# Optimization experiments

Hardware: AMD Instinct MI355X
Metric: run time of the kernel (lower is better)

The kernel has to match this reference:

```python
import jax, jax.numpy as jnp
import numpy as np

G = 7          # 7x7 feature map -> 49 nodes per image
N = G * G
K = 3          # knn_k
NEG_SLOPE = 0.2  # PyG GATConv default leaky_relu slope


def build_spatial_edges():
    # 8-neighborhood grid edges on the 7x7 map, directed (src -> dst)
    src, dst = [], []
    for r in range(G):
        for c in range(G):
            i = r * G + c
            for dr in (-1, 0, 1):
                for dc in (-1, 0, 1):
                    if dr == 0 and dc == 0:
                        continue
                    rr, cc = r + dr, c + dc
                    if 0 <= rr < G and 0 <= cc < G:
                        src.append(rr * G + cc)
                        dst.append(i)
    return np.array([src, dst], dtype=np.int32)

SPATIAL = build_spatial_edges()  # [2, 312]


def build_edges(x):
    """x: [B, N, F] node features -> (src, dst) each [B, E].
    Edges = spatial 8-neighborhood + feature-space kNN (k=3) + self-loops."""
    B = x.shape[0]
    sq = jnp.sum(x * x, axis=-1)                               # [B, N]
    d = sq[:, :, None] + sq[:, None, :] - 2.0 * jnp.einsum('bnf,bmf->bnm', x, x)
    d = d + jnp.eye(N, dtype=x.dtype) * 1e9                    # exclude self
    _, nbr = jax.lax.top_k(-d, K)                              # [B, N, K]
    knn_src = nbr.reshape(B, N * K)
    knn_dst = jnp.broadcast_to(jnp.repeat(jnp.arange(N, dtype=jnp.int32), K)[None], (B, N * K))
    sp = jnp.asarray(SPATIAL)
    Es = sp.shape[1]
    loops = jnp.arange(N, dtype=jnp.int32)
    src = jnp.concatenate([jnp.broadcast_to(sp[0][None], (B, Es)), knn_src.astype(jnp.int32),
                           jnp.broadcast_to(loops[None], (B, N))], axis=1)
    dst = jnp.concatenate([jnp.broadcast_to(sp[1][None], (B, Es)), knn_dst,
                           jnp.broadcast_to(loops[None], (B, N))], axis=1)
    return src, dst


def gat_layer(x, src, dst, W, a_src, a_dst, b, concat):
    """PyG-style GATConv (eval mode, no dropout). x: [N,F], src/dst: [E]."""
    H, C = a_src.shape
    h = (x @ W).reshape(N, H, C)                               # [N, H, C]
    es = jnp.sum(h * a_src[None], axis=-1)                     # [N, H]
    ed = jnp.sum(h * a_dst[None], axis=-1)                     # [N, H]
    e = jax.nn.leaky_relu(es[src] + ed[dst], NEG_SLOPE)        # [E, H]
    m = jax.ops.segment_max(e, dst, num_segments=N)            # [N, H]
    m = jnp.where(jnp.isfinite(m), m, 0.0)
    p = jnp.exp(e - m[dst])
    denom = jax.ops.segment_sum(p, dst, num_segments=N)
    alpha = p / jnp.maximum(denom[dst], 1e-16)                 # softmax over incoming edges
    out = jax.ops.segment_sum(alpha[:, :, None] * h[src], dst, num_segments=N)  # [N, H, C]
    out = out.reshape(N, H * C) if concat else out.mean(axis=1)
    return out + b


def setup_inputs() -> dict:
    key = jax.random.key(0)
    ks = jax.random.split(key, 14)
    B, F, Hd, Cd, O, NC = 256, 1024, 8, 128, 256, 14
    s = 0.05
    return {
        'feat_map': jax.random.normal(ks[0], (B, F, G, G), dtype=jnp.float32),
        'W1': jax.random.normal(ks[1], (F, Hd * Cd), dtype=jnp.float32) * s,
        'a_src1': jax.random.normal(ks[2], (Hd, Cd), dtype=jnp.float32) * s,
        'a_dst1': jax.random.normal(ks[3], (Hd, Cd), dtype=jnp.float32) * s,
        'b1': jnp.zeros((Hd * Cd,), dtype=jnp.float32),
        'W2': jax.random.normal(ks[4], (Hd * Cd, O), dtype=jnp.float32) * s,
        'a_src2': jax.random.normal(ks[5], (1, O), dtype=jnp.float32) * s,
        'a_dst2': jax.random.normal(ks[6], (1, O), dtype=jnp.float32) * s,
        'b2': jnp.zeros((O,), dtype=jnp.float32),
        'Wc1': jax.random.normal(ks[7], (O, O), dtype=jnp.float32) * s,
        'bc1': jnp.zeros((O,), dtype=jnp.float32),
        'Wc2': jax.random.normal(ks[8], (O, NC), dtype=jnp.float32) * s,
        'bc2': jnp.zeros((NC,), dtype=jnp.float32),
    }


def reference(feat_map, W1, a_src1, a_dst1, b1, W2, a_src2, a_dst2, b2, Wc1, bc1, Wc2, bc2):
    B = feat_map.shape[0]
    # backbone output relu + flatten 7x7 map into 49 nodes
    x = jax.nn.relu(feat_map).reshape(B, -1, N).transpose(0, 2, 1)  # [B, N, 1024]
    src, dst = build_edges(x)

    def per_graph(xg, sg, dg):
        h = jax.nn.elu(gat_layer(xg, sg, dg, W1, a_src1, a_dst1, b1, True))
        h = jax.nn.elu(gat_layer(h, sg, dg, W2, a_src2, a_dst2, b2, False))
        return h.mean(axis=0)                                   # global mean pool -> [256]

    pooled = jax.vmap(per_graph)(x, src, dst)                   # [B, 256]
    return jax.nn.relu(pooled @ Wc1 + bc1) @ Wc2 + bc2          # [B, 14]
```

## Files before the change

kernel.cpp:

```cpp
#include <hip/hip_runtime.h>

#define GDIM 7
#define NN 49
#define FDIM 1024
#define HD 8
#define CD 128
#define ODIM 256
#define NC 14
#define MAXE 12

typedef __attribute__((ext_vector_type(4))) float f32x4;
typedef __attribute__((ext_vector_type(8))) short s16x8;

struct us4 { unsigned short x, y, z, w; };

__device__ __forceinline__ unsigned short f2bf(float x) {
  unsigned u = __float_as_uint(x);
  return (unsigned short)((u + 0x7fffu + ((u >> 16) & 1u)) >> 16);
}
__device__ __forceinline__ float bf2f(unsigned short h) {
  return __uint_as_float((unsigned)h << 16);
}

#define GLOAD_LDS16(g, l)                                          \
  __builtin_amdgcn_global_load_lds(                                \
      (const __attribute__((address_space(1))) void*)(g),          \
      (__attribute__((address_space(3))) void*)(l), 16, 0, 0)

__device__ void relu_body(char* smem, int blk, const float* __restrict__ F,
                          float* __restrict__ X,
                          unsigned short* __restrict__ Xh,
                          unsigned short* __restrict__ Xl) {
  float* lds = (float*)smem;
  const int b  = blk >> 4;
  const int f0 = (blk & 15) << 6;
  const int tid = threadIdx.x;
  const float* src = F + (size_t)b * FDIM * NN + (size_t)f0 * NN;
  for (int idx = tid; idx < 64 * NN; idx += 256) lds[idx] = src[idx];
  __syncthreads();
  for (int pass = 0; pass < 13; pass++) {
    int n = pass * 4 + (tid >> 6);
    int fi = tid & 63;
    if (n < NN) {
      float v = lds[fi * NN + n];
      v = v > 0.f ? v : 0.f;
      size_t o = ((size_t)b * NN + n) * FDIM + f0 + fi;
      X[o] = v;
      unsigned short h = f2bf(v);
      Xh[o] = h;
      Xl[o] = f2bf(v - bf2f(h));
    }
  }
}

__device__ void wconvT_body(const float* __restrict__ W, int K, int N,
                            unsigned short* __restrict__ WhT,
                            unsigned short* __restrict__ WlT, int blk,
                            float* t ) {
  const int nbx = N >> 6;
  const int bx = blk % nbx, by = blk / nbx;
  const int r0 = by << 6, c0 = bx << 6;
  const int tid = threadIdx.x;
#pragma unroll
  for (int i = 0; i < 16; i++) {
    int r = i * 4 + (tid >> 6), c = tid & 63;
    t[r * 65 + c] = W[(size_t)(r0 + r) * N + c0 + c];
  }
  __syncthreads();
#pragma unroll
  for (int i = 0; i < 16; i++) {
    int n = i * 4 + (tid >> 6);
    int k = tid & 63;
    float x = t[k * 65 + n];
    unsigned short h = f2bf(x);
    size_t o = (size_t)(c0 + n) * K + r0 + k;
    WhT[o] = h;
    WlT[o] = f2bf(x - bf2f(h));
  }
}

__global__ void __launch_bounds__(256) pre_kernel(
    const float* __restrict__ F, float* __restrict__ X,
    unsigned short* __restrict__ Xh, unsigned short* __restrict__ Xl,
    const float* __restrict__ W1, unsigned short* __restrict__ W1hT,
    unsigned short* __restrict__ W1lT, const float* __restrict__ W2,
    unsigned short* __restrict__ W2hT, unsigned short* __restrict__ W2lT) {
  __shared__ __align__(16) char smem[16640];
  if (blockIdx.x < 4096) {
    relu_body(smem, blockIdx.x, F, X, Xh, Xl);
  } else if (blockIdx.x < 4352) {
    wconvT_body(W1, FDIM, FDIM, W1hT, W1lT, blockIdx.x - 4096, (float*)smem);
  } else {
    wconvT_body(W2, FDIM, ODIM, W2hT, W2lT, blockIdx.x - 4352, (float*)smem);
  }
}

__global__ void __launch_bounds__(256) knn_kernel(
    const float* __restrict__ X, int* __restrict__ srcs_g,
    int* __restrict__ cnt_g) {
  const int b = blockIdx.x, tid = threadIdx.x;
  __shared__ float xs[56][68];
  __shared__ float gram[56][57];
  const float* Xb = X + (size_t)b * NN * FDIM;

  const int tr = tid / 14, tc = tid % 14;
  float acc[4][4];
#pragma unroll
  for (int i = 0; i < 4; i++)
#pragma unroll
    for (int j = 0; j < 4; j++) acc[i][j] = 0.f;

  for (int c0 = 0; c0 < FDIM; c0 += 64) {
    __syncthreads();
    for (int idx = tid; idx < NN * 16; idx += 256) {
      int n = idx >> 4, q = idx & 15;
      *(float4*)&xs[n][q << 2] =
          *(const float4*)&Xb[(size_t)n * FDIM + c0 + (q << 2)];
    }
    __syncthreads();
    if (tid < 196) {
#pragma unroll
      for (int k4 = 0; k4 < 64; k4 += 4) {
        float4 a[4], bb[4];
#pragma unroll
        for (int i = 0; i < 4; i++) a[i]  = *(const float4*)&xs[tr + 14 * i][k4];
#pragma unroll
        for (int j = 0; j < 4; j++) bb[j] = *(const float4*)&xs[tc + 14 * j][k4];
#pragma unroll
        for (int i = 0; i < 4; i++)
#pragma unroll
          for (int j = 0; j < 4; j++)
            acc[i][j] += a[i].x * bb[j].x + a[i].y * bb[j].y +
                         a[i].z * bb[j].z + a[i].w * bb[j].w;
      }
    }
  }
  if (tid < 196) {
#pragma unroll
    for (int i = 0; i < 4; i++)
#pragma unroll
      for (int j = 0; j < 4; j++) gram[tr + 14 * i][tc + 14 * j] = acc[i][j];
  }
  __syncthreads();
  if (tid < NN) {
    const int n = tid;
    const float sqn = gram[n][n];
    float d0 = 1e30f, d1 = 1e30f, d2 = 1e30f;
    int i0 = 0, i1 = 0, i2 = 0;
    for (int m = 0; m < NN; m++) {
      if (m == n) continue;
      float d = sqn + gram[m][m] - 2.f * gram[n][m];
      if (d < d0)      { d2=d1; i2=i1; d1=d0; i1=i0; d0=d; i0=m; }
      else if (d < d1) { d2=d1; i2=i1; d1=d;  i1=m; }
      else if (d < d2) { d2=d;  i2=m; }
    }
    int srcs[MAXE];
    int r = n / GDIM, c = n % GDIM, k = 0;
    for (int dr = -1; dr <= 1; dr++)
      for (int dc = -1; dc <= 1; dc++) {
        if (dr == 0 && dc == 0) continue;
        int rr = r + dr, cc = c + dc;
        if (rr >= 0 && rr < GDIM && cc >= 0 && cc < GDIM)
          srcs[k++] = rr * GDIM + cc;
      }
    srcs[k++] = i0; srcs[k++] = i1; srcs[k++] = i2;
    srcs[k++] = n;
    cnt_g[(size_t)b * NN + n] = k;
    for (int j = 0; j < MAXE; j++)
      srcs_g[((size_t)b * NN + n) * MAXE + j] = srcs[j < k ? j : 0];
  }
}

__global__ void __launch_bounds__(256) gemm_bf16x3(
    const unsigned short* __restrict__ A_h, const unsigned short* __restrict__ A_l,
    const unsigned short* __restrict__ BT_h, const unsigned short* __restrict__ BT_l,
    float* __restrict__ C, int M, int N, int K,
    const float* __restrict__ av, const float* __restrict__ dv,
    float* __restrict__ esp, float* __restrict__ edp) {
  __shared__ unsigned short sAh[128][64], sAl[128][64];
  __shared__ unsigned short sBh[128][64], sBl[128][64];
  const int tid = threadIdx.x;
  const int w = tid >> 6, lane = tid & 63;
  const int nbx = N >> 7;
  const int nwg = gridDim.x;
  const int q = nwg >> 3, r = nwg & 7;
  const int xcd = blockIdx.x & 7, loc = blockIdx.x >> 3;
  const int wg = (xcd < r) ? (xcd * (q + 1) + loc)
                           : (r * (q + 1) + (xcd - r) * q + loc);
  const int bx = wg % nbx, by = wg / nbx;
  const int row0 = by << 7, col0 = bx << 7;
  const int wr = (w >> 1) << 6, wc = (w & 1) << 6;
  const int sgr = lane >> 3;
  const int schunk = lane & 7;
  const int fr = lane & 15;
  const int fq = lane >> 4;

  f32x4 acc[4][4];
#pragma unroll
  for (int m = 0; m < 4; m++)
#pragma unroll
    for (int n = 0; n < 4; n++) acc[m][n] = (f32x4){0.f, 0.f, 0.f, 0.f};

  for (int k0 = 0; k0 < K; k0 += 64) {
    __syncthreads();
#pragma unroll
    for (int i = 0; i < 4; i++) {
      const int rbase = (w << 5) + (i << 3);
      const int gr = rbase + sgr;
      const int sc = schunk ^ (gr & 7);
      const size_t ga = (size_t)(row0 + gr) * K + k0 + (sc << 3);
      GLOAD_LDS16(A_h + ga, &sAh[rbase][0]);
      GLOAD_LDS16(A_l + ga, &sAl[rbase][0]);
      const size_t gb = (size_t)(col0 + gr) * K + k0 + (sc << 3);
      GLOAD_LDS16(BT_h + gb, &sBh[rbase][0]);
      GLOAD_LDS16(BT_l + gb, &sBl[rbase][0]);
    }
    __syncthreads();
#pragma unroll
    for (int ks = 0; ks < 2; ks++) {
      const int cb = (ks << 2) + fq;
      s16x8 ah[4], al[4], bh[4], bl[4];
#pragma unroll
      for (int m = 0; m < 4; m++) {
        const int ra = wr + (m << 4) + fr;
        const int ca = (cb ^ (ra & 7)) << 3;
        ah[m] = *(const s16x8*)&sAh[ra][ca];
        al[m] = *(const s16x8*)&sAl[ra][ca];
        const int rb = wc + (m << 4) + fr;
        const int cbn = (cb ^ (rb & 7)) << 3;
        bh[m] = *(const s16x8*)&sBh[rb][cbn];
        bl[m] = *(const s16x8*)&sBl[rb][cbn];
      }
#pragma unroll
      for (int m = 0; m < 4; m++)
#pragma unroll
        for (int n = 0; n < 4; n++) {
          acc[m][n] = __builtin_amdgcn_mfma_f32_16x16x32_bf16(ah[m], bh[n], acc[m][n], 0, 0, 0);
          acc[m][n] = __builtin_amdgcn_mfma_f32_16x16x32_bf16(ah[m], bl[n], acc[m][n], 0, 0, 0);
          acc[m][n] = __builtin_amdgcn_mfma_f32_16x16x32_bf16(al[m], bh[n], acc[m][n], 0, 0, 0);
        }
    }
  }
  const int crow = fq << 2, ccol = fr;
#pragma unroll
  for (int m = 0; m < 4; m++)
#pragma unroll
    for (int n = 0; n < 4; n++)
#pragma unroll
      for (int v = 0; v < 4; v++)
        C[(size_t)(row0 + wr + (m << 4) + crow + v) * N + col0 + wc + (n << 4) + ccol] =
            acc[m][n][v];

  const int pstride = N >> 6;
  const int part = (col0 + wc) >> 6;
  float asv[4], adv[4];
#pragma unroll
  for (int n = 0; n < 4; n++) {
    int cidx = col0 + wc + (n << 4) + fr;
    asv[n] = av[cidx];
    adv[n] = dv[cidx];
  }
#pragma unroll
  for (int m = 0; m < 4; m++)
#pragma unroll
    for (int v = 0; v < 4; v++) {
      float s = acc[m][0][v] * asv[0] + acc[m][1][v] * asv[1] +
                acc[m][2][v] * asv[2] + acc[m][3][v] * asv[3];
      float d = acc[m][0][v] * adv[0] + acc[m][1][v] * adv[1] +
                acc[m][2][v] * adv[2] + acc[m][3][v] * adv[3];
      s += __shfl_xor(s, 1); s += __shfl_xor(s, 2);
      s += __shfl_xor(s, 4); s += __shfl_xor(s, 8);
      d += __shfl_xor(d, 1); d += __shfl_xor(d, 2);
      d += __shfl_xor(d, 4); d += __shfl_xor(d, 8);
      if (fr == 0) {
        int row = row0 + wr + (m << 4) + (fq << 2) + v;
        esp[(size_t)row * pstride + part] = s;
        edp[(size_t)row * pstride + part] = d;
      }
    }
}

__global__ void __launch_bounds__(256) attn1_agg(
    const float* __restrict__ H, const int* __restrict__ srcs_g,
    const int* __restrict__ cnt_g, const float* __restrict__ es1p,
    const float* __restrict__ ed1p, const float* __restrict__ b1,
    unsigned short* __restrict__ Zh, unsigned short* __restrict__ Zl) {
  const int bid = blockIdx.x;
  const int b = bid / NN;
  const int tid = threadIdx.x;
  __shared__ int ss[MAXE];
  __shared__ float se[MAXE][HD];
  __shared__ float edv[HD];
  __shared__ float al[MAXE][HD];
  const int k = cnt_g[bid];
  if (tid < MAXE) ss[tid] = srcs_g[(size_t)bid * MAXE + tid];
  __syncthreads();
  if (tid < MAXE * HD) {
    int j = tid >> 3, h = tid & 7;
    size_t base = ((size_t)b * NN + ss[j]) * 16 + h * 2;
    se[j][h] = es1p[base] + es1p[base + 1];
  }
  if (tid >= 128 && tid < 128 + HD) {
    int h = tid - 128;
    size_t base = (size_t)bid * 16 + h * 2;
    edv[h] = ed1p[base] + ed1p[base + 1];
  }
  __syncthreads();
  if (tid < HD) {
    const int h = tid;
    float e[MAXE];
    float m = -1e30f;
#pragma unroll
    for (int j = 0; j < MAXE; j++) {
      if (j < k) {
        float v = se[j][h] + edv[h];
        v = v >= 0.f ? v : 0.2f * v;
        e[j] = v;
        m = fmaxf(m, v);
      }
    }
    float denom = 0.f;
#pragma unroll
    for (int j = 0; j < MAXE; j++) {
      if (j < k) { e[j] = expf(e[j] - m); denom += e[j]; }
    }
    float inv = 1.f / fmaxf(denom, 1e-16f);
#pragma unroll
    for (int j = 0; j < MAXE; j++) {
      if (j < k) al[j][h] = e[j] * inv;
    }
  }
  __syncthreads();
  const float4* Hb = (const float4*)(H + (size_t)b * NN * FDIM);
  const int h = tid >> 5;
  float4 acc = ((const float4*)b1)[tid];
  for (int j = 0; j < k; j++) {
    float a = al[j][h];
    float4 v = Hb[(size_t)ss[j] * (FDIM / 4) + tid];
    acc.x += a * v.x; acc.y += a * v.y; acc.z += a * v.z; acc.w += a * v.w;
  }
  acc.x = acc.x > 0.f ? acc.x : expm1f(acc.x);
  acc.y = acc.y > 0.f ? acc.y : expm1f(acc.y);
  acc.z = acc.z > 0.f ? acc.z : expm1f(acc.z);
  acc.w = acc.w > 0.f ? acc.w : expm1f(acc.w);
  us4 hv, lv;
  hv.x = f2bf(acc.x); lv.x = f2bf(acc.x - bf2f(hv.x));
  hv.y = f2bf(acc.y); lv.y = f2bf(acc.y - bf2f(hv.y));
  hv.z = f2bf(acc.z); lv.z = f2bf(acc.z - bf2f(hv.z));
  hv.w = f2bf(acc.w); lv.w = f2bf(acc.w - bf2f(hv.w));
  *(us4*)&Zh[(size_t)bid * FDIM + (tid << 2)] = hv;
  *(us4*)&Zl[(size_t)bid * FDIM + (tid << 2)] = lv;
}

__global__ void __launch_bounds__(256) attn2_agg(
    const float* __restrict__ H2, const int* __restrict__ srcs_g,
    const int* __restrict__ cnt_g, const float* __restrict__ es2p,
    const float* __restrict__ ed2p, const float* __restrict__ b2,
    float* __restrict__ Z2) {
  const int bid = blockIdx.x;
  const int b = bid / NN;
  const int tid = threadIdx.x;
  __shared__ int ss[MAXE];
  __shared__ float se[MAXE];
  __shared__ float al[MAXE];
  const int k = cnt_g[bid];
  if (tid < MAXE) ss[tid] = srcs_g[(size_t)bid * MAXE + tid];
  __syncthreads();
  if (tid < MAXE) {
    size_t base = ((size_t)b * NN + ss[tid]) * 4;
    se[tid] = es2p[base] + es2p[base + 1] + es2p[base + 2] + es2p[base + 3];
  }
  __syncthreads();
  if (tid == 0) {
    size_t base = (size_t)bid * 4;
    float ed = ed2p[base] + ed2p[base + 1] + ed2p[base + 2] + ed2p[base + 3];
    float e[MAXE];
    float m = -1e30f;
#pragma unroll
    for (int j = 0; j < MAXE; j++) {
      if (j < k) {
        float v = se[j] + ed;
        v = v >= 0.f ? v : 0.2f * v;
        e[j] = v;
        m = fmaxf(m, v);
      }
    }
    float denom = 0.f;
#pragma unroll
    for (int j = 0; j < MAXE; j++) {
      if (j < k) { e[j] = expf(e[j] - m); denom += e[j]; }
    }
    float inv = 1.f / fmaxf(denom, 1e-16f);
#pragma unroll
    for (int j = 0; j < MAXE; j++) {
      if (j < k) al[j] = e[j] * inv;
    }
  }
  __syncthreads();
  const float* Hb = H2 + (size_t)b * NN * ODIM;
  float acc = b2[tid];
  for (int j = 0; j < k; j++)
    acc += al[j] * Hb[(size_t)ss[j] * ODIM + tid];
  acc = acc > 0.f ? acc : expm1f(acc);
  Z2[(size_t)bid * ODIM + tid] = acc;
}

__global__ void __launch_bounds__(256) classifier_kernel(
    const float* __restrict__ Z2, const float* __restrict__ Wc1,
    const float* __restrict__ bc1, const float* __restrict__ Wc2,
    const float* __restrict__ bc2, float* __restrict__ out) {
  const int b = blockIdx.x, tid = threadIdx.x;
  __shared__ float p[ODIM];
  __shared__ float t[ODIM];
  float s = 0.f;
  for (int i = 0; i < NN; i++)
    s += Z2[((size_t)b * NN + i) * ODIM + tid];
  p[tid] = s * (1.f / 49.f);
  __syncthreads();
  float a = bc1[tid];
  for (int c = 0; c < ODIM; c++) a += p[c] * Wc1[(size_t)c * ODIM + tid];
  t[tid] = a > 0.f ? a : 0.f;
  __syncthreads();
  if (tid < NC) {
    float o = bc2[tid];
    for (int j = 0; j < ODIM; j++) o += t[j] * Wc2[(size_t)j * NC + tid];
    out[(size_t)b * NC + tid] = o;
  }
}

extern "C" void kernel_launch(void* const* d_in, const int* in_sizes, int n_in,
                              void* d_out, int out_size, void* d_ws, size_t ws_size,
                              hipStream_t stream) {
  const float* feat   = (const float*)d_in[0];
  const float* W1     = (const float*)d_in[1];
  const float* a_src1 = (const float*)d_in[2];
  const float* a_dst1 = (const float*)d_in[3];
  const float* b1     = (const float*)d_in[4];
  const float* W2     = (const float*)d_in[5];
  const float* a_src2 = (const float*)d_in[6];
  const float* a_dst2 = (const float*)d_in[7];
  const float* b2     = (const float*)d_in[8];
  const float* Wc1    = (const float*)d_in[9];
  const float* bc1    = (const float*)d_in[10];
  const float* Wc2    = (const float*)d_in[11];
  const float* bc2    = (const float*)d_in[12];

  const int B = in_sizes[0] / (FDIM * NN);
  const int M = B * NN;

  const size_t xE = (size_t)M * FDIM;
  float* X  = (float*)d_ws;
  float* H1 = X + xE;
  unsigned short* Xh = (unsigned short*)(H1 + xE);
  unsigned short* Xl = Xh + xE;
  unsigned short* W1hT = Xl + xE;
  unsigned short* W1lT = W1hT + (size_t)FDIM * FDIM;
  unsigned short* W2hT = W1lT + (size_t)FDIM * FDIM;
  unsigned short* W2lT = W2hT + (size_t)ODIM * FDIM;
  int*   srcs_g = (int*)(W2lT + (size_t)ODIM * FDIM);
  int*   cnt_g  = srcs_g + (size_t)M * MAXE;
  float* es1p   = (float*)(cnt_g + M);
  float* ed1p   = es1p + (size_t)M * 16;
  float* es2p   = ed1p + (size_t)M * 16;
  float* ed2p   = es2p + (size_t)M * 4;
  float* H2  = X;
  float* Z2  = H1;
  unsigned short* Z1h = Xh;
  unsigned short* Z1l = Xl;

  const int NWG1 = (M / 128) * (FDIM / 128);
  const int NWG2 = (M / 128) * (ODIM / 128);

  pre_kernel<<<4416, 256, 0, stream>>>(feat, X, Xh, Xl, W1, W1hT, W1lT,
                                       W2, W2hT, W2lT);
  knn_kernel<<<B, 256, 0, stream>>>(X, srcs_g, cnt_g);
  gemm_bf16x3<<<NWG1, 256, 0, stream>>>(
      Xh, Xl, W1hT, W1lT, H1, M, FDIM, FDIM, a_src1, a_dst1, es1p, ed1p);
  attn1_agg<<<M, 256, 0, stream>>>(H1, srcs_g, cnt_g, es1p, ed1p, b1, Z1h, Z1l);
  gemm_bf16x3<<<NWG2, 256, 0, stream>>>(
      Z1h, Z1l, W2hT, W2lT, H2, M, ODIM, FDIM, a_src2, a_dst2, es2p, ed2p);
  attn2_agg<<<M, 256, 0, stream>>>(H2, srcs_g, cnt_g, es2p, ed2p, b2, Z2);
  classifier_kernel<<<B, 256, 0, stream>>>(Z2, Wc1, bc1, Wc2, bc2, (float*)d_out);
}
```

Before: 311.7 us.

## Split kNN Gram computation across feature chunks into partial and select kernels

The kNN Gram matrix computation, previously one block per image looping over all 1024 features, is split into four blocks per image, each covering 256 features and writing a partial Gram to workspace. A new select kernel sums the four partials and runs the top-3 neighbor selection. This raises parallelism when the batch is small relative to the CU count, at the cost of an extra kernel launch and a global round-trip for the partial Gram matrices. Summing partials in a different order may slightly change distances and could flip near-tie neighbor choices.

```diff
diff --git a/kernel.cpp b/kernel.cpp
--- a/kernel.cpp
+++ b/kernel.cpp
@@ -8,6 +8,8 @@
 #define ODIM 256
 #define NC 14
 #define MAXE 12
+#define KSPLIT 4
+#define GPSTRIDE 3192
 
 typedef __attribute__((ext_vector_type(4))) float f32x4;
 typedef __attribute__((ext_vector_type(8))) short s16x8;
@@ -95,13 +97,13 @@
   }
 }
 
-__global__ void __launch_bounds__(256) knn_kernel(
-    const float* __restrict__ X, int* __restrict__ srcs_g,
-    int* __restrict__ cnt_g) {
-  const int b = blockIdx.x, tid = threadIdx.x;
+__global__ void __launch_bounds__(256) knn_partial(
+    const float* __restrict__ X, float* __restrict__ gramP) {
+  const int gid = blockIdx.x;
+  const int b = gid >> 2, p = gid & 3;
+  const int tid = threadIdx.x;
   __shared__ float xs[56][68];
-  __shared__ float gram[56][57];
-  const float* Xb = X + (size_t)b * NN * FDIM;
+  const float* Xb = X + (size_t)b * NN * FDIM + p * 256;
 
   const int tr = tid / 14, tc = tid % 14;
   float acc[4][4];
@@ -110,7 +112,7 @@
 #pragma unroll
     for (int j = 0; j < 4; j++) acc[i][j] = 0.f;
 
-  for (int c0 = 0; c0 < FDIM; c0 += 64) {
+  for (int c0 = 0; c0 < 256; c0 += 64) {
     __syncthreads();
     for (int idx = tid; idx < NN * 16; idx += 256) {
       int n = idx >> 4, q = idx & 15;
@@ -136,10 +138,25 @@
     }
   }
   if (tid < 196) {
+    float* gp = gramP + (size_t)gid * GPSTRIDE;
 #pragma unroll
     for (int i = 0; i < 4; i++)
 #pragma unroll
-      for (int j = 0; j < 4; j++) gram[tr + 14 * i][tc + 14 * j] = acc[i][j];
+      for (int j = 0; j < 4; j++)
+        gp[(tr + 14 * i) * 57 + tc + 14 * j] = acc[i][j];
+  }
+}
+
+__global__ void __launch_bounds__(256) knn_select(
+    const float* __restrict__ gramP, int* __restrict__ srcs_g,
+    int* __restrict__ cnt_g) {
+  const int b = blockIdx.x, tid = threadIdx.x;
+  __shared__ float gram[NN][50];
+  const float* g0 = gramP + (size_t)(b * KSPLIT) * GPSTRIDE;
+  for (int idx = tid; idx < NN * NN; idx += 256) {
+    int r = idx / NN, c = idx % NN;
+    gram[r][c] = g0[r * 57 + c] + g0[GPSTRIDE + r * 57 + c] +
+                 g0[2 * GPSTRIDE + r * 57 + c] + g0[3 * GPSTRIDE + r * 57 + c];
   }
   __syncthreads();
   if (tid < NN) {
@@ -463,6 +480,7 @@
   float* ed1p   = es1p + (size_t)M * 16;
   float* es2p   = ed1p + (size_t)M * 16;
   float* ed2p   = es2p + (size_t)M * 4;
+  float* gramP  = ed2p + (size_t)M * 4;
   float* H2  = X;
   float* Z2  = H1;
   unsigned short* Z1h = Xh;
@@ -473,7 +491,8 @@
 
   pre_kernel<<<4416, 256, 0, stream>>>(feat, X, Xh, Xl, W1, W1hT, W1lT,
                                        W2, W2hT, W2lT);
-  knn_kernel<<<B, 256, 0, stream>>>(X, srcs_g, cnt_g);
+  knn_partial<<<B * KSPLIT, 256, 0, stream>>>(X, gramP);
+  knn_select<<<B, 256, 0, stream>>>(gramP, srcs_g, cnt_g);
   gemm_bf16x3<<<NWG1, 256, 0, stream>>>(
       Xh, Xl, W1hT, W1lT, H1, M, FDIM, FDIM, a_src1, a_dst1, es1p, ed1p);
   attn1_agg<<<M, 256, 0, stream>>>(H1, srcs_g, cnt_g, es1p, ed1p, b1, Z1h, Z1l);
```

New measurement: 322.3 us. 1.03x slower.

## Split kNN Gram computation across two blocks per image by row halves

Applied to the files above, without the earlier changes.

The kNN kernel now launches two blocks per image, each computing the Gram-matrix rows for one half of the nodes (28 rows) against all 49 columns. Because a block no longer holds the diagonal, squared norms are accumulated separately from the staged tile by 49 threads. This doubles block count to improve occupancy of a small-grid kernel, at the cost of each block reloading the full feature tile from global memory and some redundant norm computation.

```diff
diff --git a/kernel.cpp b/kernel.cpp
--- a/kernel.cpp
+++ b/kernel.cpp
@@ -8,6 +8,7 @@
 #define ODIM 256
 #define NC 14
 #define MAXE 12
+#define KR 28
 
 typedef __attribute__((ext_vector_type(4))) float f32x4;
 typedef __attribute__((ext_vector_type(8))) short s16x8;
@@ -98,17 +99,22 @@
 __global__ void __launch_bounds__(256) knn_kernel(
     const float* __restrict__ X, int* __restrict__ srcs_g,
     int* __restrict__ cnt_g) {
-  const int b = blockIdx.x, tid = threadIdx.x;
+  const int gid = blockIdx.x;
+  const int b = gid >> 1, p = gid & 1;
+  const int tid = threadIdx.x;
   __shared__ float xs[56][68];
-  __shared__ float gram[56][57];
+  __shared__ float gram[KR][57];
+  __shared__ float sq[NN];
   const float* Xb = X + (size_t)b * NN * FDIM;
 
   const int tr = tid / 14, tc = tid % 14;
-  float acc[4][4];
-#pragma unroll
-  for (int i = 0; i < 4; i++)
+  const int r0 = p * KR;
+  float acc[2][4];
+#pragma unroll
+  for (int i = 0; i < 2; i++)
 #pragma unroll
     for (int j = 0; j < 4; j++) acc[i][j] = 0.f;
+  float sqacc = 0.f;
 
   for (int c0 = 0; c0 < FDIM; c0 += 64) {
     __syncthreads();
@@ -121,53 +127,63 @@
     if (tid < 196) {
 #pragma unroll
       for (int k4 = 0; k4 < 64; k4 += 4) {
-        float4 a[4], bb[4];
-#pragma unroll
-        for (int i = 0; i < 4; i++) a[i]  = *(const float4*)&xs[tr + 14 * i][k4];
+        float4 a[2], bb[4];
+#pragma unroll
+        for (int i = 0; i < 2; i++) a[i]  = *(const float4*)&xs[r0 + tr + 14 * i][k4];
 #pragma unroll
         for (int j = 0; j < 4; j++) bb[j] = *(const float4*)&xs[tc + 14 * j][k4];
 #pragma unroll
-        for (int i = 0; i < 4; i++)
+        for (int i = 0; i < 2; i++)
 #pragma unroll
           for (int j = 0; j < 4; j++)
             acc[i][j] += a[i].x * bb[j].x + a[i].y * bb[j].y +
                          a[i].z * bb[j].z + a[i].w * bb[j].w;
       }
     }
+    if (tid < NN) {
+      const float* r = &xs[tid][0];
+      float s = 0.f;
+#pragma unroll 8
+      for (int j = 0; j < 64; j++) s += r[j] * r[j];
+      sqacc += s;
+    }
   }
   if (tid < 196) {
 #pragma unroll
-    for (int i = 0; i < 4; i++)
+    for (int i = 0; i < 2; i++)
 #pragma unroll
       for (int j = 0; j < 4; j++) gram[tr + 14 * i][tc + 14 * j] = acc[i][j];
   }
-  __syncthreads();
-  if (tid < NN) {
-    const int n = tid;
-    const float sqn = gram[n][n];
-    float d0 = 1e30f, d1 = 1e30f, d2 = 1e30f;
-    int i0 = 0, i1 = 0, i2 = 0;
-    for (int m = 0; m < NN; m++) {
-      if (m == n) continue;
-      float d = sqn + gram[m][m] - 2.f * gram[n][m];
-      if (d < d0)      { d2=d1; i2=i1; d1=d0; i1=i0; d0=d; i0=m; }
-      else if (d < d1) { d2=d1; i2=i1; d1=d;  i1=m; }
-      else if (d < d2) { d2=d;  i2=m; }
-    }
-    int srcs[MAXE];
-    int r = n / GDIM, c = n % GDIM, k = 0;
-    for (int dr = -1; dr <= 1; dr++)
-      for (int dc = -1; dc <= 1; dc++) {
-        if (dr == 0 && dc == 0) continue;
-        int rr = r + dr, cc = c + dc;
-        if (rr >= 0 && rr < GDIM && cc >= 0 && cc < GDIM)
-          srcs[k++] = rr * GDIM + cc;
+  if (tid < NN) sq[tid] = sqacc;
+  __syncthreads();
+  if (tid < KR) {
+    const int n = r0 + tid;
+    if (n < NN) {
+      const float sqn = sq[n];
+      float d0 = 1e30f, d1 = 1e30f, d2 = 1e30f;
+      int i0 = 0, i1 = 0, i2 = 0;
+      for (int m = 0; m < NN; m++) {
+        if (m == n) continue;
+        float d = sqn + sq[m] - 2.f * gram[tid][m];
+        if (d < d0)      { d2=d1; i2=i1; d1=d0; i1=i0; d0=d; i0=m; }
+        else if (d < d1) { d2=d1; i2=i1; d1=d;  i1=m; }
+        else if (d < d2) { d2=d;  i2=m; }
       }
-    srcs[k++] = i0; srcs[k++] = i1; srcs[k++] = i2;
-    srcs[k++] = n;
-    cnt_g[(size_t)b * NN + n] = k;
-    for (int j = 0; j < MAXE; j++)
-      srcs_g[((size_t)b * NN + n) * MAXE + j] = srcs[j < k ? j : 0];
+      int srcs[MAXE];
+      int r = n / GDIM, c = n % GDIM, k = 0;
+      for (int dr = -1; dr <= 1; dr++)
+        for (int dc = -1; dc <= 1; dc++) {
+          if (dr == 0 && dc == 0) continue;
+          int rr = r + dr, cc = c + dc;
+          if (rr >= 0 && rr < GDIM && cc >= 0 && cc < GDIM)
+            srcs[k++] = rr * GDIM + cc;
+        }
+      srcs[k++] = i0; srcs[k++] = i1; srcs[k++] = i2;
+      srcs[k++] = n;
+      cnt_g[(size_t)b * NN + n] = k;
+      for (int j = 0; j < MAXE; j++)
+        srcs_g[((size_t)b * NN + n) * MAXE + j] = srcs[j < k ? j : 0];
+    }
   }
 }
 
@@ -473,7 +489,7 @@
 
   pre_kernel<<<4416, 256, 0, stream>>>(feat, X, Xh, Xl, W1, W1hT, W1lT,
                                        W2, W2hT, W2lT);
-  knn_kernel<<<B, 256, 0, stream>>>(X, srcs_g, cnt_g);
+  knn_kernel<<<B * 2, 256, 0, stream>>>(X, srcs_g, cnt_g);
   gemm_bf16x3<<<NWG1, 256, 0, stream>>>(
       Xh, Xl, W1hT, W1lT, H1, M, FDIM, FDIM, a_src1, a_dst1, es1p, ed1p);
   attn1_agg<<<M, 256, 0, stream>>>(H1, srcs_g, cnt_g, es1p, ed1p, b1, Z1h, Z1l);
```

Result: no change. 310.9 us (median of 2 runs) (-0.2%).
